# Optimization experiments

Hardware: AMD Instinct MI355X
Metric: run time of the kernel (lower is better)

Reference implementation:

```python
import jax, jax.numpy as jnp
import numpy as np

B, C, H, W, K = 32, 64, 112, 112, 5


def setup_inputs() -> dict:
    key = jax.random.key(0)
    kx, = jax.random.split(key, 1)
    x = jax.random.uniform(kx, (B, C, H, W), dtype=jnp.float32)
    # parameters per BioNorm.reset_parameters()
    sigma = jnp.ones((C,), jnp.float32)
    pow_p = jnp.full((C,), 2.0, jnp.float32)
    sum_kernel = jnp.full((C, 1, K, K), 1.0 / (K * K), jnp.float32)
    weight = jnp.ones((C,), jnp.float32)
    bias = jnp.zeros((C,), jnp.float32)
    return {"x": x, "sigma": sigma, "pow_p": pow_p, "sum_kernel": sum_kernel,
            "weight": weight, "bias": bias}


def _bionorm(x, sigma, pow_p, sum_kernel, weight, bias):
    s = sigma.reshape(1, -1, 1, 1)
    p = pow_p.reshape(1, -1, 1, 1)
    w = weight.reshape(1, -1, 1, 1)
    b = bias.reshape(1, -1, 1, 1)
    xp = x ** p  # [B,C,H,W]
    # depthwise (grouped) conv, VALID padding -> [B,C,H-K+1,W-K+1]
    sf = jax.lax.conv_general_dilated(
        xp, sum_kernel, window_strides=(1, 1), padding='VALID',
        feature_group_count=C,
        dimension_numbers=('NCHW', 'OIHW', 'NCHW'))
    hks = K // 2
    # replicate-pad back to [B,C,H,W]
    sf = jnp.pad(sf, ((0, 0), (0, 0), (hks, hks), (hks, hks)), mode='edge')
    den = s ** p + sf
    return w * xp / den + b


def reference(x, sigma, pow_p, sum_kernel, weight, bias):
    return _bionorm(x, sigma, pow_p, sum_kernel, weight, bias)
```

## Files before the change

kernel.cpp:

```cpp
#include <hip/hip_runtime.h>


#define Cch 64
#define Hh 112
#define Ww 112
#define ST 116
#define SROWS 40
#define CPB 36
#define RPS 9

__global__ __launch_bounds__(128) void bionorm_kernel(
    const float* __restrict__ x, const float* __restrict__ sigma,
    const float* __restrict__ pow_p, const float* __restrict__ sum_kernel,
    const float* __restrict__ weight, const float* __restrict__ bias,
    float* __restrict__ out)
{
    __shared__ float lds[SROWS * ST];

    const int bx  = blockIdx.x;
    const int c   = blockIdx.y;
    const int b   = blockIdx.z;
    const int tid = threadIdx.x;

    const float p  = pow_p[c];
    const float sg = sigma[c];
    const float wc = weight[c];
    const float bc = bias[c];
    const bool  p2 = (p == 2.0f);
    const float sp = p2 ? sg * sg : __powf(sg, p);

    float kw[25];
    const float* kp = sum_kernel + c * 25;
    #pragma unroll
    for (int j = 0; j < 25; ++j) kw[j] = kp[j];

    const float* xplane = x + ((size_t)(b * Cch + c)) * (Hh * Ww);
    const int r0 = bx * CPB;

    for (int i = tid; i < SROWS * 28; i += 128) {
        int s = i / 28, q = i - s * 28;
        const float4 v = *(const float4*)(xplane + (r0 + s) * Ww + q * 4);
        float4 xp;
        if (p2) {
            xp.x = v.x * v.x; xp.y = v.y * v.y;
            xp.z = v.z * v.z; xp.w = v.w * v.w;
        } else {
            xp.x = __powf(v.x, p); xp.y = __powf(v.y, p);
            xp.z = __powf(v.z, p); xp.w = __powf(v.w, p);
        }
        *(float4*)(&lds[s * ST + q * 4]) = xp;
    }
    __syncthreads();

    const int ss = tid >> 5;
    const int g  = tid & 31;
    if (g >= 27) return;

    const int cs   = 2 + bx * CPB + ss * RPS;
    const int col0 = 4 * g;
    const int lbase = (9 * ss) * ST + col0;

    float* oplane = out + ((size_t)(b * Cch + c)) * (Hh * Ww);

    float win[5][8];

    #define LOADW(SL, KR) { \
        const float4 a_  = *(const float4*)(&lds[lbase + (KR) * ST]);     \
        const float4 b_  = *(const float4*)(&lds[lbase + (KR) * ST + 4]); \
        win[SL][0] = a_.x; win[SL][1] = a_.y; win[SL][2] = a_.z; win[SL][3] = a_.w; \
        win[SL][4] = b_.x; win[SL][5] = b_.y; win[SL][6] = b_.z; win[SL][7] = b_.w; }

    #define EMITROW(GR, SL) { \
        float* orw_ = oplane + (GR) * Ww; \
        *(float2*)(orw_ + col0 + 2) = make_float2(fmaf(wc * win[SL][2], d0, bc), \
                                                  fmaf(wc * win[SL][3], d1, bc)); \
        *(float2*)(orw_ + col0 + 4) = make_float2(fmaf(wc * win[SL][4], d2, bc), \
                                                  fmaf(wc * win[SL][5], d3, bc)); \
        if (g == 0)  *(float2*)(orw_)       = make_float2(fmaf(wc * win[SL][0], d0, bc), \
                                                          fmaf(wc * win[SL][1], d0, bc)); \
        if (g == 26) *(float2*)(orw_ + 110) = make_float2(fmaf(wc * win[SL][6], d3, bc), \
                                                          fmaf(wc * win[SL][7], d3, bc)); }

    LOADW(0, 0) LOADW(1, 1) LOADW(2, 2) LOADW(3, 3)

    #pragma unroll
    for (int k = 0; k < RPS; ++k) {
        LOADW((k + 4) % 5, k + 4)

        float S0 = 0.f, S1 = 0.f, S2 = 0.f, S3 = 0.f;
        #pragma unroll
        for (int dy = 0; dy < 5; ++dy) {
            const int sl = (k + dy) % 5;
            #pragma unroll
            for (int dx = 0; dx < 5; ++dx) {
                const float kv = kw[dy * 5 + dx];
                S0 = fmaf(kv, win[sl][dx + 0], S0);
                S1 = fmaf(kv, win[sl][dx + 1], S1);
                S2 = fmaf(kv, win[sl][dx + 2], S2);
                S3 = fmaf(kv, win[sl][dx + 3], S3);
            }
        }

        const float d0 = __builtin_amdgcn_rcpf(sp + S0);
        const float d1 = __builtin_amdgcn_rcpf(sp + S1);
        const float d2 = __builtin_amdgcn_rcpf(sp + S2);
        const float d3 = __builtin_amdgcn_rcpf(sp + S3);

        const int cgl = cs + k;
        EMITROW(cgl, (k + 2) % 5)

        if (cgl == 2) {
            EMITROW(0, (k + 0) % 5)
            EMITROW(1, (k + 1) % 5)
        }
        if (cgl == 109) {
            EMITROW(110, (k + 3) % 5)
            EMITROW(111, (k + 4) % 5)
        }
    }
    #undef LOADW
    #undef EMITROW
}

extern "C" void kernel_launch(void* const* d_in, const int* in_sizes, int n_in,
                              void* d_out, int out_size, void* d_ws, size_t ws_size,
                              hipStream_t stream) {
    const float* x          = (const float*)d_in[0];
    const float* sigma      = (const float*)d_in[1];
    const float* pow_p      = (const float*)d_in[2];
    const float* sum_kernel = (const float*)d_in[3];
    const float* weight     = (const float*)d_in[4];
    const float* bias       = (const float*)d_in[5];
    float* out = (float*)d_out;

    dim3 grid(3, Cch, 32);
    dim3 block(128);
    bionorm_kernel<<<grid, block, 0, stream>>>(x, sigma, pow_p, sum_kernel,
                                               weight, bias, out);
}
```

Measured before the change: 202.6 us.

## Replace LDS staging with direct per-thread global loads and register prefetch

Removes the shared-memory tile and its block barrier. Each thread now loads its own overlapping window rows straight from global memory, squaring or powering them in registers, and prefetches the next row one iteration ahead so the load overlaps with compute. This cuts the LDS round trip and the synchronisation, but adjacent threads now fetch overlapping columns and rows redundantly through the cache, and the rows shared between sub-slices are read several times. Edge-row emission conditions are rewritten to use compile-time k checks.

```diff
diff --git a/kernel.cpp b/kernel.cpp
--- a/kernel.cpp
+++ b/kernel.cpp
@@ -4,8 +4,6 @@
 #define Cch 64
 #define Hh 112
 #define Ww 112
-#define ST 116
-#define SROWS 40
 #define CPB 36
 #define RPS 9
 
@@ -15,12 +13,14 @@
     const float* __restrict__ weight, const float* __restrict__ bias,
     float* __restrict__ out)
 {
-    __shared__ float lds[SROWS * ST];
-
     const int bx  = blockIdx.x;
     const int c   = blockIdx.y;
     const int b   = blockIdx.z;
     const int tid = threadIdx.x;
+
+    const int ss = tid >> 5;
+    const int g  = tid & 31;
+    if (g >= 27) return;
 
     const float p  = pow_p[c];
     const float sg = sigma[c];
@@ -35,40 +35,25 @@
     for (int j = 0; j < 25; ++j) kw[j] = kp[j];
 
     const float* xplane = x + ((size_t)(b * Cch + c)) * (Hh * Ww);
-    const int r0 = bx * CPB;
-
-    for (int i = tid; i < SROWS * 28; i += 128) {
-        int s = i / 28, q = i - s * 28;
-        const float4 v = *(const float4*)(xplane + (r0 + s) * Ww + q * 4);
-        float4 xp;
-        if (p2) {
-            xp.x = v.x * v.x; xp.y = v.y * v.y;
-            xp.z = v.z * v.z; xp.w = v.w * v.w;
-        } else {
-            xp.x = __powf(v.x, p); xp.y = __powf(v.y, p);
-            xp.z = __powf(v.z, p); xp.w = __powf(v.w, p);
-        }
-        *(float4*)(&lds[s * ST + q * 4]) = xp;
-    }
-    __syncthreads();
-
-    const int ss = tid >> 5;
-    const int g  = tid & 31;
-    if (g >= 27) return;
+    float* oplane = out + ((size_t)(b * Cch + c)) * (Hh * Ww);
 
     const int cs   = 2 + bx * CPB + ss * RPS;
     const int col0 = 4 * g;
-    const int lbase = (9 * ss) * ST + col0;
-
-    float* oplane = out + ((size_t)(b * Cch + c)) * (Hh * Ww);
 
     float win[5][8];
 
-    #define LOADW(SL, KR) { \
-        const float4 a_  = *(const float4*)(&lds[lbase + (KR) * ST]);     \
-        const float4 b_  = *(const float4*)(&lds[lbase + (KR) * ST + 4]); \
-        win[SL][0] = a_.x; win[SL][1] = a_.y; win[SL][2] = a_.z; win[SL][3] = a_.w; \
-        win[SL][4] = b_.x; win[SL][5] = b_.y; win[SL][6] = b_.z; win[SL][7] = b_.w; }
+    #define CVT8(SL, VA, VB) { \
+        if (p2) { \
+            win[SL][0] = VA.x * VA.x; win[SL][1] = VA.y * VA.y; \
+            win[SL][2] = VA.z * VA.z; win[SL][3] = VA.w * VA.w; \
+            win[SL][4] = VB.x * VB.x; win[SL][5] = VB.y * VB.y; \
+            win[SL][6] = VB.z * VB.z; win[SL][7] = VB.w * VB.w; \
+        } else { \
+            win[SL][0] = __powf(VA.x, p); win[SL][1] = __powf(VA.y, p); \
+            win[SL][2] = __powf(VA.z, p); win[SL][3] = __powf(VA.w, p); \
+            win[SL][4] = __powf(VB.x, p); win[SL][5] = __powf(VB.y, p); \
+            win[SL][6] = __powf(VB.z, p); win[SL][7] = __powf(VB.w, p); \
+        } }
 
     #define EMITROW(GR, SL) { \
         float* orw_ = oplane + (GR) * Ww; \
@@ -81,11 +66,28 @@
         if (g == 26) *(float2*)(orw_ + 110) = make_float2(fmaf(wc * win[SL][6], d3, bc), \
                                                           fmaf(wc * win[SL][7], d3, bc)); }
 
-    LOADW(0, 0) LOADW(1, 1) LOADW(2, 2) LOADW(3, 3)
+    {
+        const float4 a0 = *(const float4*)(xplane + (cs - 2) * Ww + col0);
+        const float4 b0 = *(const float4*)(xplane + (cs - 2) * Ww + col0 + 4);
+        const float4 a1 = *(const float4*)(xplane + (cs - 1) * Ww + col0);
+        const float4 b1 = *(const float4*)(xplane + (cs - 1) * Ww + col0 + 4);
+        const float4 a2 = *(const float4*)(xplane + (cs    ) * Ww + col0);
+        const float4 b2 = *(const float4*)(xplane + (cs    ) * Ww + col0 + 4);
+        const float4 a3 = *(const float4*)(xplane + (cs + 1) * Ww + col0);
+        const float4 b3 = *(const float4*)(xplane + (cs + 1) * Ww + col0 + 4);
+        CVT8(0, a0, b0) CVT8(1, a1, b1) CVT8(2, a2, b2) CVT8(3, a3, b3)
+    }
+    float4 A0 = *(const float4*)(xplane + (cs + 2) * Ww + col0);
+    float4 A1 = *(const float4*)(xplane + (cs + 2) * Ww + col0 + 4);
 
     #pragma unroll
     for (int k = 0; k < RPS; ++k) {
-        LOADW((k + 4) % 5, k + 4)
+        const int nr  = cs + k + 3;
+        const int nrc = nr > 111 ? 111 : nr;
+        const float4 B0 = *(const float4*)(xplane + nrc * Ww + col0);
+        const float4 B1 = *(const float4*)(xplane + nrc * Ww + col0 + 4);
+
+        CVT8((k + 4) % 5, A0, A1)
 
         float S0 = 0.f, S1 = 0.f, S2 = 0.f, S3 = 0.f;
         #pragma unroll
@@ -109,16 +111,18 @@
         const int cgl = cs + k;
         EMITROW(cgl, (k + 2) % 5)
 
-        if (cgl == 2) {
-            EMITROW(0, (k + 0) % 5)
-            EMITROW(1, (k + 1) % 5)
+        if (k == 0 && cs == 2) {
+            EMITROW(0, 0)
+            EMITROW(1, 1)
         }
-        if (cgl == 109) {
+        if (k == RPS - 1 && cgl == 109) {
             EMITROW(110, (k + 3) % 5)
             EMITROW(111, (k + 4) % 5)
         }
+
+        A0 = B0; A1 = B1;
     }
-    #undef LOADW
+    #undef CVT8
     #undef EMITROW
 }
 
```

Result: no change. 199.0 us (-1.8%).
